# Kernel optimization log

Hardware: AMD Instinct MI355X
Metric: run time of the kernel (lower is better)

The kernel has to match this reference:

```python
import jax, jax.numpy as jnp
import numpy as np

TEMPERATURE = 8.0  # sqrt(d_k) with d_k = 64
NEG_INF = -jnp.inf


def setup_inputs() -> dict:
    key = jax.random.key(0)
    kq, kk, kv = jax.random.split(key, 3)
    b, n, d = 16, 2048, 64
    q = jax.random.normal(kq, (b, n, d), dtype=jnp.float32)
    k = jax.random.normal(kk, (b, n, d), dtype=jnp.float32)
    v = jax.random.normal(kv, (b, n, d), dtype=jnp.float32)
    # causal mask: True where attention is disallowed (strict upper triangle)
    mask = jnp.broadcast_to(jnp.triu(jnp.ones((n, n), dtype=bool), k=1), (b, n, n))
    return {"q": q, "k": k, "v": v, "mask": mask}


def reference(q, k, v, mask):
    # attn = q @ k^T / temperature   [b, n, n]
    attn = jnp.einsum('bqd,bkd->bqk', q, k) / TEMPERATURE
    attn = jnp.where(mask, NEG_INF, attn)
    attn = jax.nn.softmax(attn, axis=2)
    # output = attn @ v   [b, n, d]
    output = jnp.einsum('bqk,bkd->bqd', attn, v)
    return (output, attn)
```

## Files before the change

kernel.cpp:

```cpp
#include <hip/hip_runtime.h>


constexpr int B = 16;
constexpr int N = 2048;
constexpr int D = 64;
constexpr float INV_TEMP = 0.125f;

typedef __attribute__((ext_vector_type(8))) short bf16x8;
typedef __attribute__((ext_vector_type(4))) float f32x4;

__device__ __forceinline__ short f2bf(float f) {
    __bf16 h = (__bf16)f;
    return __builtin_bit_cast(short, h);
}

__global__ __launch_bounds__(512) void sdpa_fused2(
    const float* __restrict__ q,
    const float* __restrict__ k,
    const float* __restrict__ v,
    float* __restrict__ out,
    float* __restrict__ attn)
{
    __shared__ __align__(16) short sK[2][64][72];
    __shared__ __align__(16) short sV[2][64][72];
    __shared__ __align__(16) short sPt[32][72];
    __shared__ float rsum[128];
    __shared__ float sinv[32];

    const int x   = blockIdx.x;
    const int xcd = x & 7;
    const int idx = x >> 3;
    const int b   = xcd * 2 + (idx & 1);
    const int u   = idx >> 1;

    const int t    = threadIdx.x;
    const int w    = t >> 6;
    const int lane = t & 63;
    const int l15  = lane & 15;
    const int quad = lane >> 4;
    const int q8   = quad * 8;
    const int rg   = w & 1;
    const int cg   = w >> 1;

    const float* qb = q + (size_t)b * N * D;
    const float* kb = k + (size_t)b * N * D;
    const float* vb = v + (size_t)b * N * D;
    float* attn_b = attn + (size_t)b * N * N;

    const int krow = t >> 3;
    const int kc8  = (t & 7) * 8;

    for (int h = 0; h < 2; ++h) {
        const int rt = h ? u : (63 - u);
        const int qs = rt * 32;
        const int nt = (rt >> 1) + 1;

        float4 kf0, kf1;
        float  vr[8];
        {
            const float4* s = (const float4*)(kb + (size_t)krow * D + kc8);
            kf0 = s[0]; kf1 = s[1];
            const float* sv = vb + (size_t)(w * 8) * D + lane;
#pragma unroll
            for (int i = 0; i < 8; ++i) vr[i] = sv[(size_t)i * D];
        }

        __syncthreads();
        if (t < 256) {
            const float4* s = (const float4*)(qb + (size_t)(qs + krow) * D + kc8);
            float4 a = s[0], c4 = s[1];
            float qv[8] = {a.x,a.y,a.z,a.w, c4.x,c4.y,c4.z,c4.w};
            bf16x8 pq;
#pragma unroll
            for (int i = 0; i < 8; ++i) pq[i] = f2bf(qv[i]);
            *(bf16x8*)&sPt[krow][kc8] = pq;
        }
        __syncthreads();
        const bf16x8 qa0 = *(const bf16x8*)&sPt[rg * 16 + l15][q8];
        const bf16x8 qa1 = *(const bf16x8*)&sPt[rg * 16 + l15][32 + q8];

        float rs[4] = {0.f, 0.f, 0.f, 0.f};
        f32x4 o = {0.f, 0.f, 0.f, 0.f};

        for (int kt = 0; kt < nt; ++kt) {
            const int cur = kt & 1;
            {
                float kv[8] = {kf0.x,kf0.y,kf0.z,kf0.w, kf1.x,kf1.y,kf1.z,kf1.w};
                bf16x8 pk, pv;
#pragma unroll
                for (int i = 0; i < 8; ++i) pk[i] = f2bf(kv[i]);
#pragma unroll
                for (int i = 0; i < 8; ++i) pv[i] = f2bf(vr[i]);
                *(bf16x8*)&sK[cur][krow][kc8]  = pk;
                *(bf16x8*)&sV[cur][lane][w*8]  = pv;
            }
            __syncthreads();
            if (kt + 1 < nt) {
                const float4* s = (const float4*)(kb + (size_t)((kt+1)*64 + krow) * D + kc8);
                kf0 = s[0]; kf1 = s[1];
                const float* sv = vb + (size_t)((kt+1)*64 + w*8) * D + lane;
#pragma unroll
                for (int i = 0; i < 8; ++i) vr[i] = sv[(size_t)i * D];
            }
            bf16x8 b0 = *(const bf16x8*)&sK[cur][cg * 16 + l15][q8];
            bf16x8 b1 = *(const bf16x8*)&sK[cur][cg * 16 + l15][32 + q8];
            f32x4 c = {0.f, 0.f, 0.f, 0.f};
            c = __builtin_amdgcn_mfma_f32_16x16x32_bf16(qa0, b0, c, 0, 0, 0);
            c = __builtin_amdgcn_mfma_f32_16x16x32_bf16(qa1, b1, c, 0, 0, 0);
            const int colg = kt * 64 + cg * 16 + l15;
#pragma unroll
            for (int r = 0; r < 4; ++r) {
                const int rowg = qs + rg * 16 + quad * 4 + r;
                float pr = (colg <= rowg) ? __expf(c[r] * INV_TEMP) : 0.f;
                rs[r] += pr;
                sPt[rg * 16 + quad * 4 + r][cg * 16 + l15] = f2bf(pr);
            }
            __syncthreads();
#pragma unroll
            for (int kc = 0; kc < 2; ++kc) {
                bf16x8 a  = *(const bf16x8*)&sPt[rg * 16 + l15][kc * 32 + q8];
                bf16x8 vf = *(const bf16x8*)&sV[cur][cg * 16 + l15][kc * 32 + q8];
                o = __builtin_amdgcn_mfma_f32_16x16x32_bf16(a, vf, o, 0, 0, 0);
            }
        }

#pragma unroll
        for (int r = 0; r < 4; ++r) {
            float s = rs[r];
            s += __shfl_xor(s, 1);
            s += __shfl_xor(s, 2);
            s += __shfl_xor(s, 4);
            s += __shfl_xor(s, 8);
            rs[r] = s;
        }
        if (l15 == 0) {
#pragma unroll
            for (int r = 0; r < 4; ++r) rsum[w * 16 + quad * 4 + r] = rs[r];
        }
        __syncthreads();
        if (t < 32) {
            const int rg2 = t >> 4, rl = t & 15;
            float tot = rsum[(rg2 + 0) * 16 + rl] + rsum[(rg2 + 2) * 16 + rl]
                      + rsum[(rg2 + 4) * 16 + rl] + rsum[(rg2 + 6) * 16 + rl];
            sinv[t] = 1.f / tot;
        }
        __syncthreads();

#pragma unroll
        for (int r = 0; r < 4; ++r) {
            const int rowl = rg * 16 + quad * 4 + r;
            out[(size_t)(b * N + qs + rowl) * D + cg * 16 + l15] = o[r] * sinv[rowl];
        }

        const int qrow = qs + rg * 16 + l15;
        const float einv = sinv[rg * 16 + l15];
        float* arow = attn_b + (size_t)qrow * N;

        float4 ka0, ka1, ka2, ka3;
        {
            const float* kr = kb + (size_t)(cg * 16 + l15) * D;
            const float4* kp = (const float4*)(kr + q8);
            ka0 = kp[0]; ka1 = kp[1];
            const float4* kp2 = (const float4*)(kr + 32 + q8);
            ka2 = kp2[0]; ka3 = kp2[1];
        }
        for (int kt = 0; kt < nt; ++kt) {
            float kv[16] = {ka0.x,ka0.y,ka0.z,ka0.w, ka1.x,ka1.y,ka1.z,ka1.w,
                            ka2.x,ka2.y,ka2.z,ka2.w, ka3.x,ka3.y,ka3.z,ka3.w};
            bf16x8 kb0, kb1;
#pragma unroll
            for (int i = 0; i < 8; ++i) { kb0[i] = f2bf(kv[i]); kb1[i] = f2bf(kv[8 + i]); }
            if (kt + 1 < nt) {
                const float* kr = kb + (size_t)((kt+1)*64 + cg * 16 + l15) * D;
                const float4* kp = (const float4*)(kr + q8);
                ka0 = kp[0]; ka1 = kp[1];
                const float4* kp2 = (const float4*)(kr + 32 + q8);
                ka2 = kp2[0]; ka3 = kp2[1];
            }
            f32x4 c = {0.f, 0.f, 0.f, 0.f};
            c = __builtin_amdgcn_mfma_f32_16x16x32_bf16(kb0, qa0, c, 0, 0, 0);
            c = __builtin_amdgcn_mfma_f32_16x16x32_bf16(kb1, qa1, c, 0, 0, 0);

            const int kg0 = kt * 64 + cg * 16 + quad * 4;
            float4 pv4;
            pv4.x = (kg0 + 0 <= qrow) ? __expf(c[0] * INV_TEMP) * einv : 0.f;
            pv4.y = (kg0 + 1 <= qrow) ? __expf(c[1] * INV_TEMP) * einv : 0.f;
            pv4.z = (kg0 + 2 <= qrow) ? __expf(c[2] * INV_TEMP) * einv : 0.f;
            pv4.w = (kg0 + 3 <= qrow) ? __expf(c[3] * INV_TEMP) * einv : 0.f;
            *(float4*)(arow + kg0) = pv4;
        }

        const int lim  = nt * 64;
        const int erow = t >> 4;
        const int ec   = (t & 15) * 4;
        float* zrow = attn_b + (size_t)(qs + erow) * N;
        const float4 z = {0.f, 0.f, 0.f, 0.f};
        for (int c0 = lim + ec; c0 < N; c0 += 64) {
            *(float4*)(zrow + c0) = z;
        }
    }
}

extern "C" void kernel_launch(void* const* d_in, const int* in_sizes, int n_in,
                              void* d_out, int out_size, void* d_ws, size_t ws_size,
                              hipStream_t stream) {
    const float* q = (const float*)d_in[0];
    const float* k = (const float*)d_in[1];
    const float* v = (const float*)d_in[2];

    float* out  = (float*)d_out;
    float* attn = out + (size_t)B * N * D;

    sdpa_fused2<<<dim3(B * 32), dim3(512), 0, stream>>>(q, k, v, out, attn);
}
```

Before: 471.6 us.

## Interleave first tile's attention-matrix writeback with second tile's flash pass

Restructures the per-block two-tile schedule so that the attention-probability recomputation and store for the first query tile run inside the second tile's flash loop, spread across its iterations. The separate zero-fill loop is folded into the per-tile stream, which now writes zeros for fully masked column tiles. The order of heavy and light row tiles is also alternated across blocks via an xor of block index bits. The aim is to overlap the large global attention-matrix writes with MFMA and LDS work rather than leaving them as a serial tail. In exchange, K loads for the streamed tiles are no longer software-prefetched, register pressure rises, and the interleaved stores may contend with the flash loop's loads.

```diff
diff --git a/kernel.cpp b/kernel.cpp
--- a/kernel.cpp
+++ b/kernel.cpp
@@ -14,7 +14,7 @@
     return __builtin_bit_cast(short, h);
 }
 
-__global__ __launch_bounds__(512) void sdpa_fused2(
+__global__ __launch_bounds__(512) void sdpa_fused3(
     const float* __restrict__ q,
     const float* __restrict__ k,
     const float* __restrict__ v,
@@ -25,13 +25,17 @@
     __shared__ __align__(16) short sV[2][64][72];
     __shared__ __align__(16) short sPt[32][72];
     __shared__ float rsum[128];
-    __shared__ float sinv[32];
+    __shared__ float sinv2[2][32];
 
     const int x   = blockIdx.x;
     const int xcd = x & 7;
     const int idx = x >> 3;
     const int b   = xcd * 2 + (idx & 1);
     const int u   = idx >> 1;
+    const int hf  = ((x >> 3) ^ (x >> 8)) & 1;
+
+    const int rtA = hf ? (63 - u) : u;
+    const int rtB = hf ? u : (63 - u);
 
     const int t    = threadIdx.x;
     const int w    = t >> 6;
@@ -50,10 +54,40 @@
     const int krow = t >> 3;
     const int kc8  = (t & 7) * 8;
 
-    for (int h = 0; h < 2; ++h) {
-        const int rt = h ? u : (63 - u);
-        const int qs = rt * 32;
-        const int nt = (rt >> 1) + 1;
+    auto stream_tile = [&](int ct, bf16x8 a0, bf16x8 a1, float einv,
+                           int qrow, int rmax, float* arow) {
+        const int c0  = ct * 64 + cg * 16;
+        const int kg0 = c0 + quad * 4;
+        float4 pv4;
+        if (c0 <= rmax) {
+            const float* kr = kb + (size_t)(c0 + l15) * D;
+            const float4* kp = (const float4*)(kr + q8);
+            float4 k0 = kp[0], k1 = kp[1];
+            const float4* kp2 = (const float4*)(kr + 32 + q8);
+            float4 k2 = kp2[0], k3 = kp2[1];
+            float kv[16] = {k0.x,k0.y,k0.z,k0.w, k1.x,k1.y,k1.z,k1.w,
+                            k2.x,k2.y,k2.z,k2.w, k3.x,k3.y,k3.z,k3.w};
+            bf16x8 kb0, kb1;
+#pragma unroll
+            for (int i = 0; i < 8; ++i) { kb0[i] = f2bf(kv[i]); kb1[i] = f2bf(kv[8 + i]); }
+            f32x4 c = {0.f, 0.f, 0.f, 0.f};
+            c = __builtin_amdgcn_mfma_f32_16x16x32_bf16(kb0, a0, c, 0, 0, 0);
+            c = __builtin_amdgcn_mfma_f32_16x16x32_bf16(kb1, a1, c, 0, 0, 0);
+            pv4.x = (kg0 + 0 <= qrow) ? __expf(c[0] * INV_TEMP) * einv : 0.f;
+            pv4.y = (kg0 + 1 <= qrow) ? __expf(c[1] * INV_TEMP) * einv : 0.f;
+            pv4.z = (kg0 + 2 <= qrow) ? __expf(c[2] * INV_TEMP) * einv : 0.f;
+            pv4.w = (kg0 + 3 <= qrow) ? __expf(c[3] * INV_TEMP) * einv : 0.f;
+        } else {
+            pv4 = {0.f, 0.f, 0.f, 0.f};
+        }
+        *(float4*)(arow + kg0) = pv4;
+    };
+
+    auto flash = [&](int rt, int slot, bf16x8& qa0o, bf16x8& qa1o,
+                     bool inter, bf16x8 sa0, bf16x8 sa1, float seinv,
+                     int sqrow, int srmax, float* sarow) {
+        const int qs_ = rt * 32;
+        const int nt  = (rt >> 1) + 1;
 
         float4 kf0, kf1;
         float  vr[8];
@@ -67,7 +101,7 @@
 
         __syncthreads();
         if (t < 256) {
-            const float4* s = (const float4*)(qb + (size_t)(qs + krow) * D + kc8);
+            const float4* s = (const float4*)(qb + (size_t)(qs_ + krow) * D + kc8);
             float4 a = s[0], c4 = s[1];
             float qv[8] = {a.x,a.y,a.z,a.w, c4.x,c4.y,c4.z,c4.w};
             bf16x8 pq;
@@ -78,9 +112,11 @@
         __syncthreads();
         const bf16x8 qa0 = *(const bf16x8*)&sPt[rg * 16 + l15][q8];
         const bf16x8 qa1 = *(const bf16x8*)&sPt[rg * 16 + l15][32 + q8];
+        qa0o = qa0; qa1o = qa1;
 
         float rs[4] = {0.f, 0.f, 0.f, 0.f};
         f32x4 o = {0.f, 0.f, 0.f, 0.f};
+        int sc = 0;
 
         for (int kt = 0; kt < nt; ++kt) {
             const int cur = kt & 1;
@@ -110,10 +146,15 @@
             const int colg = kt * 64 + cg * 16 + l15;
 #pragma unroll
             for (int r = 0; r < 4; ++r) {
-                const int rowg = qs + rg * 16 + quad * 4 + r;
+                const int rowg = qs_ + rg * 16 + quad * 4 + r;
                 float pr = (colg <= rowg) ? __expf(c[r] * INV_TEMP) : 0.f;
                 rs[r] += pr;
                 sPt[rg * 16 + quad * 4 + r][cg * 16 + l15] = f2bf(pr);
+            }
+            if (inter) {
+                const int se = (32 * (kt + 1)) / nt;
+                for (; sc < se; ++sc)
+                    stream_tile(sc, sa0, sa1, seinv, sqrow, srmax, sarow);
             }
             __syncthreads();
 #pragma unroll
@@ -142,63 +183,35 @@
             const int rg2 = t >> 4, rl = t & 15;
             float tot = rsum[(rg2 + 0) * 16 + rl] + rsum[(rg2 + 2) * 16 + rl]
                       + rsum[(rg2 + 4) * 16 + rl] + rsum[(rg2 + 6) * 16 + rl];
-            sinv[t] = 1.f / tot;
+            sinv2[slot][t] = 1.f / tot;
         }
         __syncthreads();
 
 #pragma unroll
         for (int r = 0; r < 4; ++r) {
             const int rowl = rg * 16 + quad * 4 + r;
-            out[(size_t)(b * N + qs + rowl) * D + cg * 16 + l15] = o[r] * sinv[rowl];
-        }
-
-        const int qrow = qs + rg * 16 + l15;
-        const float einv = sinv[rg * 16 + l15];
-        float* arow = attn_b + (size_t)qrow * N;
-
-        float4 ka0, ka1, ka2, ka3;
-        {
-            const float* kr = kb + (size_t)(cg * 16 + l15) * D;
-            const float4* kp = (const float4*)(kr + q8);
-            ka0 = kp[0]; ka1 = kp[1];
-            const float4* kp2 = (const float4*)(kr + 32 + q8);
-            ka2 = kp2[0]; ka3 = kp2[1];
-        }
-        for (int kt = 0; kt < nt; ++kt) {
-            float kv[16] = {ka0.x,ka0.y,ka0.z,ka0.w, ka1.x,ka1.y,ka1.z,ka1.w,
-                            ka2.x,ka2.y,ka2.z,ka2.w, ka3.x,ka3.y,ka3.z,ka3.w};
-            bf16x8 kb0, kb1;
-#pragma unroll
-            for (int i = 0; i < 8; ++i) { kb0[i] = f2bf(kv[i]); kb1[i] = f2bf(kv[8 + i]); }
-            if (kt + 1 < nt) {
-                const float* kr = kb + (size_t)((kt+1)*64 + cg * 16 + l15) * D;
-                const float4* kp = (const float4*)(kr + q8);
-                ka0 = kp[0]; ka1 = kp[1];
-                const float4* kp2 = (const float4*)(kr + 32 + q8);
-                ka2 = kp2[0]; ka3 = kp2[1];
-            }
-            f32x4 c = {0.f, 0.f, 0.f, 0.f};
-            c = __builtin_amdgcn_mfma_f32_16x16x32_bf16(kb0, qa0, c, 0, 0, 0);
-            c = __builtin_amdgcn_mfma_f32_16x16x32_bf16(kb1, qa1, c, 0, 0, 0);
-
-            const int kg0 = kt * 64 + cg * 16 + quad * 4;
-            float4 pv4;
-            pv4.x = (kg0 + 0 <= qrow) ? __expf(c[0] * INV_TEMP) * einv : 0.f;
-            pv4.y = (kg0 + 1 <= qrow) ? __expf(c[1] * INV_TEMP) * einv : 0.f;
-            pv4.z = (kg0 + 2 <= qrow) ? __expf(c[2] * INV_TEMP) * einv : 0.f;
-            pv4.w = (kg0 + 3 <= qrow) ? __expf(c[3] * INV_TEMP) * einv : 0.f;
-            *(float4*)(arow + kg0) = pv4;
-        }
-
-        const int lim  = nt * 64;
-        const int erow = t >> 4;
-        const int ec   = (t & 15) * 4;
-        float* zrow = attn_b + (size_t)(qs + erow) * N;
-        const float4 z = {0.f, 0.f, 0.f, 0.f};
-        for (int c0 = lim + ec; c0 < N; c0 += 64) {
-            *(float4*)(zrow + c0) = z;
-        }
-    }
+            out[(size_t)(b * N + qs_ + rowl) * D + cg * 16 + l15]
+                = o[r] * sinv2[slot][rowl];
+        }
+    };
+
+    bf16x8 qaA0, qaA1, qaB0, qaB1;
+    bf16x8 dummy = {};
+    flash(rtA, 0, qaA0, qaA1, false, dummy, dummy, 0.f, 0, 0, nullptr);
+
+    const float einvA = sinv2[0][rg * 16 + l15];
+    const int   qrowA = rtA * 32 + rg * 16 + l15;
+    const int   rmaxA = rtA * 32 + rg * 16 + 15;
+    float* arowA = attn_b + (size_t)qrowA * N;
+
+    flash(rtB, 1, qaB0, qaB1, true, qaA0, qaA1, einvA, qrowA, rmaxA, arowA);
+
+    const float einvB = sinv2[1][rg * 16 + l15];
+    const int   qrowB = rtB * 32 + rg * 16 + l15;
+    const int   rmaxB = rtB * 32 + rg * 16 + 15;
+    float* arowB = attn_b + (size_t)qrowB * N;
+    for (int ct = 0; ct < 32; ++ct)
+        stream_tile(ct, qaB0, qaB1, einvB, qrowB, rmaxB, arowB);
 }
 
 extern "C" void kernel_launch(void* const* d_in, const int* in_sizes, int n_in,
@@ -211,5 +224,5 @@
     float* out  = (float*)d_out;
     float* attn = out + (size_t)B * N * D;
 
-    sdpa_fused2<<<dim3(B * 32), dim3(512), 0, stream>>>(q, k, v, out, attn);
+    sdpa_fused3<<<dim3(B * 32), dim3(512), 0, stream>>>(q, k, v, out, attn);
 }
```

Result: no change. 476.5 us (+1.0%).

## Split into row-sum pre-pass and single-pass normalized attention plus PV kernel

Applied to the files above, without the earlier changes.

Splits the work into two kernels. The first computes the softmax row sums and zero-fills the masked upper triangle with nontemporal stores. The second then computes QK^T once per tile, writes the already-normalized probabilities straight to attn, and uses the same values for the PV product, so the output needs no final rescaling. This removes the old second QK^T pass inside the fused kernel, but QK^T is still computed twice overall, now across two launches, and the row inverses make a round trip through workspace. It also changes the Q fragment loads to go directly from global memory and alternates block ordering with an hf bit to balance load.

```diff
diff --git a/kernel.cpp b/kernel.cpp
--- a/kernel.cpp
+++ b/kernel.cpp
@@ -7,31 +7,31 @@
 constexpr float INV_TEMP = 0.125f;
 
 typedef __attribute__((ext_vector_type(8))) short bf16x8;
+typedef __attribute__((ext_vector_type(4))) short bf16x4;
 typedef __attribute__((ext_vector_type(4))) float f32x4;
 
 __device__ __forceinline__ short f2bf(float f) {
     __bf16 h = (__bf16)f;
     return __builtin_bit_cast(short, h);
 }
-
-__global__ __launch_bounds__(512) void sdpa_fused2(
+__device__ __forceinline__ void nts4(float* p, f32x4 v) {
+    __builtin_nontemporal_store(v, (f32x4*)p);
+}
+
+__global__ __launch_bounds__(512) void sdpa_rowsum(
     const float* __restrict__ q,
     const float* __restrict__ k,
-    const float* __restrict__ v,
-    float* __restrict__ out,
+    float* __restrict__ invws,
     float* __restrict__ attn)
 {
-    __shared__ __align__(16) short sK[2][64][72];
-    __shared__ __align__(16) short sV[2][64][72];
-    __shared__ __align__(16) short sPt[32][72];
-    __shared__ float rsum[128];
-    __shared__ float sinv[32];
+    __shared__ float rsum[8][16];
 
     const int x   = blockIdx.x;
     const int xcd = x & 7;
     const int idx = x >> 3;
     const int b   = xcd * 2 + (idx & 1);
     const int u   = idx >> 1;
+    const int hf  = ((x >> 3) ^ (x >> 8)) & 1;
 
     const int t    = threadIdx.x;
     const int w    = t >> 6;
@@ -44,6 +44,108 @@
 
     const float* qb = q + (size_t)b * N * D;
     const float* kb = k + (size_t)b * N * D;
+    float* attn_b = attn + (size_t)b * N * N;
+
+    for (int h = 0; h < 2; ++h) {
+        const int rt  = (h ^ hf) ? (63 - u) : u;
+        const int qs  = rt * 32;
+        const int ntl = (rt >> 1) + 1;
+
+        {
+            const int lim = ntl * 64, erow = t >> 4, ec = (t & 15) * 4;
+            float* zrow = attn_b + (size_t)(qs + erow) * N;
+            const f32x4 z = {0.f, 0.f, 0.f, 0.f};
+            for (int c0 = lim + ec; c0 < N; c0 += 64) nts4(zrow + c0, z);
+        }
+
+        const int qrow = qs + rg * 16 + l15;
+        bf16x8 qa0, qa1;
+        {
+            const float* qr = qb + (size_t)qrow * D;
+            const float4* p0 = (const float4*)(qr + q8);
+            float4 a = p0[0], bq = p0[1];
+            const float4* p1 = (const float4*)(qr + 32 + q8);
+            float4 c4 = p1[0], d4 = p1[1];
+            float qv[16] = {a.x,a.y,a.z,a.w, bq.x,bq.y,bq.z,bq.w,
+                            c4.x,c4.y,c4.z,c4.w, d4.x,d4.y,d4.z,d4.w};
+#pragma unroll
+            for (int i = 0; i < 8; ++i) { qa0[i] = f2bf(qv[i]); qa1[i] = f2bf(qv[8+i]); }
+        }
+
+        float rsacc = 0.f;
+        float4 ka0, ka1, ka2, ka3;
+        {
+            const float* kr = kb + (size_t)(cg * 16 + l15) * D;
+            const float4* p0 = (const float4*)(kr + q8);
+            ka0 = p0[0]; ka1 = p0[1];
+            const float4* p1 = (const float4*)(kr + 32 + q8);
+            ka2 = p1[0]; ka3 = p1[1];
+        }
+        for (int kt = 0; kt < ntl; ++kt) {
+            float kv[16] = {ka0.x,ka0.y,ka0.z,ka0.w, ka1.x,ka1.y,ka1.z,ka1.w,
+                            ka2.x,ka2.y,ka2.z,ka2.w, ka3.x,ka3.y,ka3.z,ka3.w};
+            bf16x8 kb0, kb1;
+#pragma unroll
+            for (int i = 0; i < 8; ++i) { kb0[i] = f2bf(kv[i]); kb1[i] = f2bf(kv[8+i]); }
+            if (kt + 1 < ntl) {
+                const float* kr = kb + (size_t)((kt+1)*64 + cg * 16 + l15) * D;
+                const float4* p0 = (const float4*)(kr + q8);
+                ka0 = p0[0]; ka1 = p0[1];
+                const float4* p1 = (const float4*)(kr + 32 + q8);
+                ka2 = p1[0]; ka3 = p1[1];
+            }
+            f32x4 c = {0.f, 0.f, 0.f, 0.f};
+            c = __builtin_amdgcn_mfma_f32_16x16x32_bf16(kb0, qa0, c, 0, 0, 0);
+            c = __builtin_amdgcn_mfma_f32_16x16x32_bf16(kb1, qa1, c, 0, 0, 0);
+            const int kg0 = kt * 64 + cg * 16 + quad * 4;
+#pragma unroll
+            for (int r = 0; r < 4; ++r)
+                if (kg0 + r <= qrow) rsacc += __expf(c[r] * INV_TEMP);
+        }
+        rsacc += __shfl_xor(rsacc, 16);
+        rsacc += __shfl_xor(rsacc, 32);
+        if (lane < 16) rsum[w][l15] = rsacc;
+        __syncthreads();
+        if (t < 32) {
+            const int rr = t >> 4, rl = t & 15;
+            float tot = rsum[rr][rl] + rsum[rr + 2][rl]
+                      + rsum[rr + 4][rl] + rsum[rr + 6][rl];
+            invws[(size_t)b * N + qs + t] = 1.f / tot;
+        }
+        __syncthreads();
+    }
+}
+
+__global__ __launch_bounds__(512) void sdpa_main(
+    const float* __restrict__ q,
+    const float* __restrict__ k,
+    const float* __restrict__ v,
+    const float* __restrict__ invws,
+    float* __restrict__ out,
+    float* __restrict__ attn)
+{
+    __shared__ __align__(16) short sK[2][64][72];
+    __shared__ __align__(16) short sV[2][64][72];
+    __shared__ __align__(16) short sPt[32][72];
+
+    const int x   = blockIdx.x;
+    const int xcd = x & 7;
+    const int idx = x >> 3;
+    const int b   = xcd * 2 + (idx & 1);
+    const int u   = idx >> 1;
+    const int hf  = ((x >> 3) ^ (x >> 8)) & 1;
+
+    const int t    = threadIdx.x;
+    const int w    = t >> 6;
+    const int lane = t & 63;
+    const int l15  = lane & 15;
+    const int quad = lane >> 4;
+    const int q8   = quad * 8;
+    const int rg   = w & 1;
+    const int cg   = w >> 1;
+
+    const float* qb = q + (size_t)b * N * D;
+    const float* kb = k + (size_t)b * N * D;
     const float* vb = v + (size_t)b * N * D;
     float* attn_b = attn + (size_t)b * N * N;
 
@@ -51,9 +153,25 @@
     const int kc8  = (t & 7) * 8;
 
     for (int h = 0; h < 2; ++h) {
-        const int rt = h ? u : (63 - u);
-        const int qs = rt * 32;
-        const int nt = (rt >> 1) + 1;
+        const int rt  = (h ^ hf) ? (63 - u) : u;
+        const int qs  = rt * 32;
+        const int ntl = (rt >> 1) + 1;
+
+        const int qrow = qs + rg * 16 + l15;
+        bf16x8 qa0, qa1;
+        {
+            const float* qr = qb + (size_t)qrow * D;
+            const float4* p0 = (const float4*)(qr + q8);
+            float4 a = p0[0], bq = p0[1];
+            const float4* p1 = (const float4*)(qr + 32 + q8);
+            float4 c4 = p1[0], d4 = p1[1];
+            float qv[16] = {a.x,a.y,a.z,a.w, bq.x,bq.y,bq.z,bq.w,
+                            c4.x,c4.y,c4.z,c4.w, d4.x,d4.y,d4.z,d4.w};
+#pragma unroll
+            for (int i = 0; i < 8; ++i) { qa0[i] = f2bf(qv[i]); qa1[i] = f2bf(qv[8+i]); }
+        }
+        const float einv = invws[(size_t)b * N + qrow];
+        float* arow = attn_b + (size_t)qrow * N;
 
         float4 kf0, kf1;
         float  vr[8];
@@ -65,24 +183,10 @@
             for (int i = 0; i < 8; ++i) vr[i] = sv[(size_t)i * D];
         }
 
+        f32x4 o = {0.f, 0.f, 0.f, 0.f};
         __syncthreads();
-        if (t < 256) {
-            const float4* s = (const float4*)(qb + (size_t)(qs + krow) * D + kc8);
-            float4 a = s[0], c4 = s[1];
-            float qv[8] = {a.x,a.y,a.z,a.w, c4.x,c4.y,c4.z,c4.w};
-            bf16x8 pq;
-#pragma unroll
-            for (int i = 0; i < 8; ++i) pq[i] = f2bf(qv[i]);
-            *(bf16x8*)&sPt[krow][kc8] = pq;
-        }
-        __syncthreads();
-        const bf16x8 qa0 = *(const bf16x8*)&sPt[rg * 16 + l15][q8];
-        const bf16x8 qa1 = *(const bf16x8*)&sPt[rg * 16 + l15][32 + q8];
-
-        float rs[4] = {0.f, 0.f, 0.f, 0.f};
-        f32x4 o = {0.f, 0.f, 0.f, 0.f};
-
-        for (int kt = 0; kt < nt; ++kt) {
+
+        for (int kt = 0; kt < ntl; ++kt) {
             const int cur = kt & 1;
             {
                 float kv[8] = {kf0.x,kf0.y,kf0.z,kf0.w, kf1.x,kf1.y,kf1.z,kf1.w};
@@ -91,30 +195,33 @@
                 for (int i = 0; i < 8; ++i) pk[i] = f2bf(kv[i]);
 #pragma unroll
                 for (int i = 0; i < 8; ++i) pv[i] = f2bf(vr[i]);
-                *(bf16x8*)&sK[cur][krow][kc8]  = pk;
-                *(bf16x8*)&sV[cur][lane][w*8]  = pv;
+                *(bf16x8*)&sK[cur][krow][kc8] = pk;
+                *(bf16x8*)&sV[cur][lane][w*8] = pv;
             }
             __syncthreads();
-            if (kt + 1 < nt) {
+            if (kt + 1 < ntl) {
                 const float4* s = (const float4*)(kb + (size_t)((kt+1)*64 + krow) * D + kc8);
                 kf0 = s[0]; kf1 = s[1];
                 const float* sv = vb + (size_t)((kt+1)*64 + w*8) * D + lane;
 #pragma unroll
                 for (int i = 0; i < 8; ++i) vr[i] = sv[(size_t)i * D];
             }
-            bf16x8 b0 = *(const bf16x8*)&sK[cur][cg * 16 + l15][q8];
-            bf16x8 b1 = *(const bf16x8*)&sK[cur][cg * 16 + l15][32 + q8];
+            bf16x8 ka0 = *(const bf16x8*)&sK[cur][cg * 16 + l15][q8];
+            bf16x8 ka1 = *(const bf16x8*)&sK[cur][cg * 16 + l15][32 + q8];
             f32x4 c = {0.f, 0.f, 0.f, 0.f};
-            c = __builtin_amdgcn_mfma_f32_16x16x32_bf16(qa0, b0, c, 0, 0, 0);
-            c = __builtin_amdgcn_mfma_f32_16x16x32_bf16(qa1, b1, c, 0, 0, 0);
-            const int colg = kt * 64 + cg * 16 + l15;
+            c = __builtin_amdgcn_mfma_f32_16x16x32_bf16(ka0, qa0, c, 0, 0, 0);
+            c = __builtin_amdgcn_mfma_f32_16x16x32_bf16(ka1, qa1, c, 0, 0, 0);
+            const int kg0 = kt * 64 + cg * 16 + quad * 4;
+            f32x4 pv4;
+            bf16x4 pb;
 #pragma unroll
             for (int r = 0; r < 4; ++r) {
-                const int rowg = qs + rg * 16 + quad * 4 + r;
-                float pr = (colg <= rowg) ? __expf(c[r] * INV_TEMP) : 0.f;
-                rs[r] += pr;
-                sPt[rg * 16 + quad * 4 + r][cg * 16 + l15] = f2bf(pr);
-            }
+                float pr = (kg0 + r <= qrow) ? __expf(c[r] * INV_TEMP) * einv : 0.f;
+                pv4[r] = pr;
+                pb[r]  = f2bf(pr);
+            }
+            nts4(arow + kg0, pv4);
+            *(bf16x4*)&sPt[rg * 16 + l15][cg * 16 + quad * 4] = pb;
             __syncthreads();
 #pragma unroll
             for (int kc = 0; kc < 2; ++kc) {
@@ -126,77 +233,7 @@
 
 #pragma unroll
         for (int r = 0; r < 4; ++r) {
-            float s = rs[r];
-            s += __shfl_xor(s, 1);
-            s += __shfl_xor(s, 2);
-            s += __shfl_xor(s, 4);
-            s += __shfl_xor(s, 8);
-            rs[r] = s;
-        }
-        if (l15 == 0) {
-#pragma unroll
-            for (int r = 0; r < 4; ++r) rsum[w * 16 + quad * 4 + r] = rs[r];
-        }
-        __syncthreads();
-        if (t < 32) {
-            const int rg2 = t >> 4, rl = t & 15;
-            float tot = rsum[(rg2 + 0) * 16 + rl] + rsum[(rg2 + 2) * 16 + rl]
-                      + rsum[(rg2 + 4) * 16 + rl] + rsum[(rg2 + 6) * 16 + rl];
-            sinv[t] = 1.f / tot;
-        }
-        __syncthreads();
-
-#pragma unroll
-        for (int r = 0; r < 4; ++r) {
-            const int rowl = rg * 16 + quad * 4 + r;
-            out[(size_t)(b * N + qs + rowl) * D + cg * 16 + l15] = o[r] * sinv[rowl];
-        }
-
-        const int qrow = qs + rg * 16 + l15;
-        const float einv = sinv[rg * 16 + l15];
-        float* arow = attn_b + (size_t)qrow * N;
-
-        float4 ka0, ka1, ka2, ka3;
-        {
-            const float* kr = kb + (size_t)(cg * 16 + l15) * D;
-            const float4* kp = (const float4*)(kr + q8);
-            ka0 = kp[0]; ka1 = kp[1];
-            const float4* kp2 = (const float4*)(kr + 32 + q8);
-            ka2 = kp2[0]; ka3 = kp2[1];
-        }
-        for (int kt = 0; kt < nt; ++kt) {
-            float kv[16] = {ka0.x,ka0.y,ka0.z,ka0.w, ka1.x,ka1.y,ka1.z,ka1.w,
-                            ka2.x,ka2.y,ka2.z,ka2.w, ka3.x,ka3.y,ka3.z,ka3.w};
-            bf16x8 kb0, kb1;
-#pragma unroll
-            for (int i = 0; i < 8; ++i) { kb0[i] = f2bf(kv[i]); kb1[i] = f2bf(kv[8 + i]); }
-            if (kt + 1 < nt) {
-                const float* kr = kb + (size_t)((kt+1)*64 + cg * 16 + l15) * D;
-                const float4* kp = (const float4*)(kr + q8);
-                ka0 = kp[0]; ka1 = kp[1];
-                const float4* kp2 = (const float4*)(kr + 32 + q8);
-                ka2 = kp2[0]; ka3 = kp2[1];
-            }
-            f32x4 c = {0.f, 0.f, 0.f, 0.f};
-            c = __builtin_amdgcn_mfma_f32_16x16x32_bf16(kb0, qa0, c, 0, 0, 0);
-            c = __builtin_amdgcn_mfma_f32_16x16x32_bf16(kb1, qa1, c, 0, 0, 0);
-
-            const int kg0 = kt * 64 + cg * 16 + quad * 4;
-            float4 pv4;
-            pv4.x = (kg0 + 0 <= qrow) ? __expf(c[0] * INV_TEMP) * einv : 0.f;
-            pv4.y = (kg0 + 1 <= qrow) ? __expf(c[1] * INV_TEMP) * einv : 0.f;
-            pv4.z = (kg0 + 2 <= qrow) ? __expf(c[2] * INV_TEMP) * einv : 0.f;
-            pv4.w = (kg0 + 3 <= qrow) ? __expf(c[3] * INV_TEMP) * einv : 0.f;
-            *(float4*)(arow + kg0) = pv4;
-        }
-
-        const int lim  = nt * 64;
-        const int erow = t >> 4;
-        const int ec   = (t & 15) * 4;
-        float* zrow = attn_b + (size_t)(qs + erow) * N;
-        const float4 z = {0.f, 0.f, 0.f, 0.f};
-        for (int c0 = lim + ec; c0 < N; c0 += 64) {
-            *(float4*)(zrow + c0) = z;
+            out[(size_t)(b * N + qs + rg * 16 + quad * 4 + r) * D + cg * 16 + l15] = o[r];
         }
     }
 }
@@ -210,6 +247,8 @@
 
     float* out  = (float*)d_out;
     float* attn = out + (size_t)B * N * D;
-
-    sdpa_fused2<<<dim3(B * 32), dim3(512), 0, stream>>>(q, k, v, out, attn);
-}
+    float* invws = (float*)d_ws;
+
+    sdpa_rowsum<<<dim3(B * 32), dim3(512), 0, stream>>>(q, k, invws, attn);
+    sdpa_main  <<<dim3(B * 32), dim3(512), 0, stream>>>(q, k, v, invws, out, attn);
+}
```

Measured after the change: 534.3 us. +13.3%, slower.

## Pre-convert Q/K/V to bf16 in workspace with transposed V before fused attention

Applied to the files above, without the earlier changes.

Adds a pre-pass kernel that converts Q and K to bf16 and writes V transposed in bf16 into the workspace. The main kernel then loads bf16 operands directly, which halves input traffic and removes per-tile conversions. The attention-probability write pass now uses nontemporal stores and writes the zero region in the same per-row loop, with the half-order alternated per block for load balance. The cost is an extra kernel launch and a workspace round trip; the original kernel is kept as a fallback when the workspace is too small.

```diff
diff --git a/kernel.cpp b/kernel.cpp
--- a/kernel.cpp
+++ b/kernel.cpp
@@ -13,8 +13,218 @@
     __bf16 h = (__bf16)f;
     return __builtin_bit_cast(short, h);
 }
-
-__global__ __launch_bounds__(512) void sdpa_fused2(
+__device__ __forceinline__ void nts4(float* p, f32x4 v) {
+    __builtin_nontemporal_store(v, (f32x4*)p);
+}
+
+__global__ __launch_bounds__(256) void cvt_inputs(
+    const float* __restrict__ q,
+    const float* __restrict__ k,
+    const float* __restrict__ v,
+    short* __restrict__ qbf,
+    short* __restrict__ kbf,
+    short* __restrict__ vbft)
+{
+    __shared__ float lds[64][65];
+
+    const int x = blockIdx.x;
+    const int t = threadIdx.x;
+
+    {
+        const size_t g = ((size_t)x * 256 + t) * 16;
+        const float4* qs4 = (const float4*)(q + g);
+        const float4* ks4 = (const float4*)(k + g);
+        float4 a0 = qs4[0], a1 = qs4[1], a2 = qs4[2], a3 = qs4[3];
+        float4 b0 = ks4[0], b1 = ks4[1], b2 = ks4[2], b3 = ks4[3];
+        float qv[16] = {a0.x,a0.y,a0.z,a0.w, a1.x,a1.y,a1.z,a1.w,
+                        a2.x,a2.y,a2.z,a2.w, a3.x,a3.y,a3.z,a3.w};
+        float kv[16] = {b0.x,b0.y,b0.z,b0.w, b1.x,b1.y,b1.z,b1.w,
+                        b2.x,b2.y,b2.z,b2.w, b3.x,b3.y,b3.z,b3.w};
+        bf16x8 q0, q1, k0, k1;
+#pragma unroll
+        for (int i = 0; i < 8; ++i) {
+            q0[i] = f2bf(qv[i]);     q1[i] = f2bf(qv[8 + i]);
+            k0[i] = f2bf(kv[i]);     k1[i] = f2bf(kv[8 + i]);
+        }
+        *(bf16x8*)(qbf + g)     = q0;
+        *(bf16x8*)(qbf + g + 8) = q1;
+        *(bf16x8*)(kbf + g)     = k0;
+        *(bf16x8*)(kbf + g + 8) = k1;
+    }
+
+    const int b  = x >> 5;
+    const int nc = x & 31;
+    const float* vt = v + ((size_t)b * N + nc * 64) * D;
+    {
+        const int r  = t >> 2;
+        const int c0 = (t & 3) * 16;
+        const float4* s = (const float4*)(vt + (size_t)r * D + c0);
+        float4 f0 = s[0], f1 = s[1], f2 = s[2], f3 = s[3];
+        float fv[16] = {f0.x,f0.y,f0.z,f0.w, f1.x,f1.y,f1.z,f1.w,
+                        f2.x,f2.y,f2.z,f2.w, f3.x,f3.y,f3.z,f3.w};
+#pragma unroll
+        for (int i = 0; i < 16; ++i) lds[r][c0 + i] = fv[i];
+    }
+    __syncthreads();
+    {
+        const int d  = t >> 2;
+        const int c0 = (t & 3) * 16;
+        bf16x8 o0, o1;
+#pragma unroll
+        for (int j = 0; j < 8; ++j) {
+            o0[j] = f2bf(lds[c0 + j][d]);
+            o1[j] = f2bf(lds[c0 + 8 + j][d]);
+        }
+        short* dst = vbft + ((size_t)b * D + d) * N + nc * 64 + c0;
+        *(bf16x8*)dst       = o0;
+        *(bf16x8*)(dst + 8) = o1;
+    }
+}
+
+__global__ __launch_bounds__(512) void sdpa_fused4(
+    const short* __restrict__ qbf,
+    const short* __restrict__ kbf,
+    const short* __restrict__ vbft,
+    float* __restrict__ out,
+    float* __restrict__ attn)
+{
+    __shared__ __align__(16) short sK[2][64][72];
+    __shared__ __align__(16) short sV[2][64][72];
+    __shared__ __align__(16) short sPt[32][72];
+    __shared__ float rsum[128];
+    __shared__ float sinv[32];
+
+    const int x   = blockIdx.x;
+    const int xcd = x & 7;
+    const int idx = x >> 3;
+    const int b   = xcd * 2 + (idx & 1);
+    const int u   = idx >> 1;
+    const int hf  = ((x >> 3) ^ (x >> 8)) & 1;
+
+    const int t    = threadIdx.x;
+    const int w    = t >> 6;
+    const int lane = t & 63;
+    const int l15  = lane & 15;
+    const int quad = lane >> 4;
+    const int q8   = quad * 8;
+    const int rg   = w & 1;
+    const int cg   = w >> 1;
+
+    const short* qbb = qbf + (size_t)b * N * D;
+    const short* kbb = kbf + (size_t)b * N * D;
+    const short* vbb = vbft + (size_t)b * D * N;
+    float* attn_b = attn + (size_t)b * N * N;
+
+    const int krow = t >> 3;
+    const int kc8  = (t & 7) * 8;
+    const int vd   = t >> 3;
+    const int vk8  = (t & 7) * 8;
+
+    for (int h = 0; h < 2; ++h) {
+        const int rt  = (h ^ hf) ? (63 - u) : u;
+        const int qs  = rt * 32;
+        const int ntl = (rt >> 1) + 1;
+
+        const int qrow = qs + rg * 16 + l15;
+        const bf16x8 qa0 = *(const bf16x8*)&qbb[(size_t)qrow * D + q8];
+        const bf16x8 qa1 = *(const bf16x8*)&qbb[(size_t)qrow * D + 32 + q8];
+
+        bf16x8 kf = *(const bf16x8*)&kbb[(size_t)krow * D + kc8];
+        bf16x8 vf = *(const bf16x8*)&vbb[(size_t)vd * N + vk8];
+
+        float rs[4] = {0.f, 0.f, 0.f, 0.f};
+        f32x4 o = {0.f, 0.f, 0.f, 0.f};
+
+        __syncthreads();
+
+        for (int kt = 0; kt < ntl; ++kt) {
+            const int cur = kt & 1;
+            *(bf16x8*)&sK[cur][krow][kc8] = kf;
+            *(bf16x8*)&sV[cur][vd][vk8]   = vf;
+            __syncthreads();
+            if (kt + 1 < ntl) {
+                kf = *(const bf16x8*)&kbb[(size_t)((kt+1)*64 + krow) * D + kc8];
+                vf = *(const bf16x8*)&vbb[(size_t)vd * N + (kt+1)*64 + vk8];
+            }
+            bf16x8 b0 = *(const bf16x8*)&sK[cur][cg * 16 + l15][q8];
+            bf16x8 b1 = *(const bf16x8*)&sK[cur][cg * 16 + l15][32 + q8];
+            f32x4 c = {0.f, 0.f, 0.f, 0.f};
+            c = __builtin_amdgcn_mfma_f32_16x16x32_bf16(qa0, b0, c, 0, 0, 0);
+            c = __builtin_amdgcn_mfma_f32_16x16x32_bf16(qa1, b1, c, 0, 0, 0);
+            const int colg = kt * 64 + cg * 16 + l15;
+#pragma unroll
+            for (int r = 0; r < 4; ++r) {
+                const int rowg = qs + rg * 16 + quad * 4 + r;
+                float pr = (colg <= rowg) ? __expf(c[r] * INV_TEMP) : 0.f;
+                rs[r] += pr;
+                sPt[rg * 16 + quad * 4 + r][cg * 16 + l15] = f2bf(pr);
+            }
+            __syncthreads();
+#pragma unroll
+            for (int kc = 0; kc < 2; ++kc) {
+                bf16x8 a  = *(const bf16x8*)&sPt[rg * 16 + l15][kc * 32 + q8];
+                bf16x8 vv = *(const bf16x8*)&sV[cur][cg * 16 + l15][kc * 32 + q8];
+                o = __builtin_amdgcn_mfma_f32_16x16x32_bf16(a, vv, o, 0, 0, 0);
+            }
+        }
+
+#pragma unroll
+        for (int r = 0; r < 4; ++r) {
+            float s = rs[r];
+            s += __shfl_xor(s, 1);
+            s += __shfl_xor(s, 2);
+            s += __shfl_xor(s, 4);
+            s += __shfl_xor(s, 8);
+            rs[r] = s;
+        }
+        if (l15 == 0) {
+#pragma unroll
+            for (int r = 0; r < 4; ++r) rsum[w * 16 + quad * 4 + r] = rs[r];
+        }
+        __syncthreads();
+        if (t < 32) {
+            const int rr = t >> 4, rl = t & 15;
+            float tot = rsum[(rr + 0) * 16 + rl] + rsum[(rr + 2) * 16 + rl]
+                      + rsum[(rr + 4) * 16 + rl] + rsum[(rr + 6) * 16 + rl];
+            sinv[t] = 1.f / tot;
+        }
+        __syncthreads();
+
+#pragma unroll
+        for (int r = 0; r < 4; ++r) {
+            const int rowl = rg * 16 + quad * 4 + r;
+            out[(size_t)(b * N + qs + rowl) * D + cg * 16 + l15]
+                = o[r] * sinv[rowl];
+        }
+
+        const float einv = sinv[rg * 16 + l15];
+        const int   rmax = qs + rg * 16 + 15;
+        float* arow = attn_b + (size_t)qrow * N;
+
+        for (int ct = 0; ct < 32; ++ct) {
+            const int c0  = ct * 64 + cg * 16;
+            const int kg0 = c0 + quad * 4;
+            f32x4 pv4;
+            if (c0 <= rmax) {
+                const short* krb = kbb + (size_t)(c0 + l15) * D;
+                bf16x8 kb0 = *(const bf16x8*)(krb + q8);
+                bf16x8 kb1 = *(const bf16x8*)(krb + 32 + q8);
+                f32x4 c = {0.f, 0.f, 0.f, 0.f};
+                c = __builtin_amdgcn_mfma_f32_16x16x32_bf16(kb0, qa0, c, 0, 0, 0);
+                c = __builtin_amdgcn_mfma_f32_16x16x32_bf16(kb1, qa1, c, 0, 0, 0);
+                pv4.x = (kg0 + 0 <= qrow) ? __expf(c[0] * INV_TEMP) * einv : 0.f;
+                pv4.y = (kg0 + 1 <= qrow) ? __expf(c[1] * INV_TEMP) * einv : 0.f;
+                pv4.z = (kg0 + 2 <= qrow) ? __expf(c[2] * INV_TEMP) * einv : 0.f;
+                pv4.w = (kg0 + 3 <= qrow) ? __expf(c[3] * INV_TEMP) * einv : 0.f;
+            } else {
+                pv4 = {0.f, 0.f, 0.f, 0.f};
+            }
+            nts4(arow + kg0, pv4);
+        }
+    }
+}
+
+__global__ __launch_bounds__(512) void sdpa_fused2_fb(
     const float* __restrict__ q,
     const float* __restrict__ k,
     const float* __restrict__ v,
@@ -139,9 +349,9 @@
         }
         __syncthreads();
         if (t < 32) {
-            const int rg2 = t >> 4, rl = t & 15;
-            float tot = rsum[(rg2 + 0) * 16 + rl] + rsum[(rg2 + 2) * 16 + rl]
-                      + rsum[(rg2 + 4) * 16 + rl] + rsum[(rg2 + 6) * 16 + rl];
+            const int rr = t >> 4, rl = t & 15;
+            float tot = rsum[(rr + 0) * 16 + rl] + rsum[(rr + 2) * 16 + rl]
+                      + rsum[(rr + 4) * 16 + rl] + rsum[(rr + 6) * 16 + rl];
             sinv[t] = 1.f / tot;
         }
         __syncthreads();
@@ -211,5 +421,16 @@
     float* out  = (float*)d_out;
     float* attn = out + (size_t)B * N * D;
 
-    sdpa_fused2<<<dim3(B * 32), dim3(512), 0, stream>>>(q, k, v, out, attn);
-}
+    const size_t elems = (size_t)B * N * D;
+    const size_t need  = elems * 3 * sizeof(short);
+
+    if (d_ws != nullptr && ws_size >= need) {
+        short* qbf  = (short*)d_ws;
+        short* kbf  = qbf + elems;
+        short* vbft = kbf + elems;
+        cvt_inputs<<<dim3(512), dim3(256), 0, stream>>>(q, k, v, qbf, kbf, vbft);
+        sdpa_fused4<<<dim3(B * 32), dim3(512), 0, stream>>>(qbf, kbf, vbft, out, attn);
+    } else {
+        sdpa_fused2_fb<<<dim3(B * 32), dim3(512), 0, stream>>>(q, k, v, out, attn);
+    }
+}
```

After: 469.6 us. No clear change (-0.4%).
